# Kernel optimization log

Measured on AMD Instinct MI355X. Metric: run time of the kernel, lower is better.

## Reference

```python
import jax, jax.numpy as jnp
import numpy as np

HIDDEN = 4096
N_HEADS = 32
HEAD_DIM = HIDDEN // N_HEADS  # 128, rotary_dim == head_dim
ROPE_BASE = 10000.0


def apply_rope(x, positions):
    # x: [B, S, n_heads, head_dim]; positions: [B, S] int. GPT-NeoX style (half split).
    hd = x.shape[-1]
    inv_freq = 1.0 / (ROPE_BASE ** (jnp.arange(0, hd, 2, dtype=jnp.float32) / hd))
    freqs = positions.astype(jnp.float32)[..., None] * inv_freq  # [B, S, hd/2]
    cos = jnp.cos(freqs)[:, :, None, :]  # [B, S, 1, hd/2]
    sin = jnp.sin(freqs)[:, :, None, :]
    x1, x2 = jnp.split(x, 2, axis=-1)
    return jnp.concatenate([x1 * cos - x2 * sin, x2 * cos + x1 * sin], axis=-1)


def setup_inputs() -> dict:
    key = jax.random.key(0)
    k1, k2, k3 = jax.random.split(key, 3)
    B, S = 2, 2048
    hidden_states = jax.random.normal(k1, (B, S, HIDDEN), dtype=jnp.float32)
    positions = jnp.broadcast_to(jnp.arange(S, dtype=jnp.int32), (B, S))
    # nn.Linear(hidden, 3*hidden, bias=False): weight [3*hidden, hidden]
    W_pack = jax.random.normal(k2, (3 * HIDDEN, HIDDEN), dtype=jnp.float32) * (HIDDEN ** -0.5)
    W_o = jax.random.normal(k3, (HIDDEN, HIDDEN), dtype=jnp.float32) * (HIDDEN ** -0.5)
    return {"hidden_states": hidden_states, "positions": positions, "W_pack": W_pack, "W_o": W_o}


def reference(hidden_states, positions, W_pack, W_o):
    B, S, H = hidden_states.shape
    scale = HEAD_DIM ** -0.5
    proj = hidden_states @ W_pack.T            # [B, S, 3H]
    q, k, v = jnp.split(proj, 3, axis=-1)
    q = q.reshape(B, S, N_HEADS, HEAD_DIM)
    k = k.reshape(B, S, N_HEADS, HEAD_DIM)
    v = v.reshape(B, S, N_HEADS, HEAD_DIM)
    q = apply_rope(q, positions)
    k = apply_rope(k, positions)
    scores = jnp.einsum("bqnd,bknd->bnqk", q, k) * scale  # [B, n, S, S]
    causal = jnp.tril(jnp.ones((S, S), dtype=bool))
    scores = jnp.where(causal, scores, jnp.finfo(scores.dtype).min)
    probs = jax.nn.softmax(scores, axis=-1)
    attn = jnp.einsum("bnqk,bknd->bqnd", probs, v).reshape(B, S, H)
    return attn @ W_o.T
```

## Files before the change

### kernel.cpp

```cpp
#include <hip/hip_runtime.h>
#include <stdint.h>

#define HIDDEN 4096
#define NHEADS 32
#define HD 128
#define SEQ 2048
#define NTOK 4096
#define QKVN 12288

typedef __attribute__((ext_vector_type(8))) short frag8;
typedef __attribute__((ext_vector_type(4))) float fl4;

__device__ __forceinline__ unsigned short f2b(float f) {
    unsigned u = __float_as_uint(f);
    return (unsigned short)((u + 0x7FFFu + ((u >> 16) & 1u)) >> 16);
}
__device__ __forceinline__ float b2f(unsigned short h) {
    return __uint_as_float(((unsigned)h) << 16);
}
__device__ __forceinline__ void gl_lds16(const void* g, void* l) {
    __builtin_amdgcn_global_load_lds(
        (const __attribute__((address_space(1))) unsigned int*)(uintptr_t)g,
        (__attribute__((address_space(3))) unsigned int*)(uintptr_t)l,
        16, 0, 0);
}

__global__ void cvt_f32_bf16(const float* __restrict__ src,
                             unsigned short* __restrict__ dst, int n8) {
    int i = blockIdx.x * 256 + threadIdx.x;
    if (i >= n8) return;
    long e = (long)i * 8;
    fl4 a = *(const fl4*)(src + e);
    fl4 b = *(const fl4*)(src + e + 4);
    union { unsigned short us[8]; frag8 v; } o;
    o.us[0] = f2b(a[0]); o.us[1] = f2b(a[1]); o.us[2] = f2b(a[2]); o.us[3] = f2b(a[3]);
    o.us[4] = f2b(b[0]); o.us[5] = f2b(b[1]); o.us[6] = f2b(b[2]); o.us[7] = f2b(b[3]);
    *(frag8*)(dst + e) = o.v;
}

__global__ void rope_kernel(unsigned short* __restrict__ proj,
                            const int* __restrict__ positions) {
    int tid = blockIdx.x * 256 + threadIdx.x;
    int j  = tid & 63;
    int h  = (tid >> 6) & 31;
    int qk = (tid >> 11) & 1;
    int t  = tid >> 12;
    int pos = positions[t];
    float inv = __builtin_amdgcn_exp2f(-0.20762051f * (float)j);
    float fr = (float)pos * inv;
    float sv = __sinf(fr), cv = __cosf(fr);
    unsigned short* base = proj + (long)t * QKVN + qk * HIDDEN + h * HD;
    float x1 = b2f(base[j]);
    float x2 = b2f(base[j + 64]);
    base[j]      = f2b(x1 * cv - x2 * sv);
    base[j + 64] = f2b(x2 * cv + x1 * sv);
}

template <int OUT_F32>
__global__ __launch_bounds__(512, 2) void gemm256(
    const unsigned short* __restrict__ A,
    const unsigned short* __restrict__ B,
    void* __restrict__ Cv, int M, int N, int K) {
    __shared__ unsigned short lds[65536];
    const int tid = threadIdx.x, lane = tid & 63, w = tid >> 6;
    const int wr = w >> 2, wc = w & 3;
    const int fr = lane & 15, quad = lane >> 4;

    const int gx = gridDim.x;
    const int nwg = gx * gridDim.y;
    int bid = blockIdx.y * gx + blockIdx.x;
    const int cpx = nwg >> 3;
    int swz = (bid & 7) * cpx + (bid >> 3);
    const long n0 = (long)(swz % gx) * 256;
    const long m0 = (long)(swz / gx) * 256;

    const int r0 = w * 8 + (lane >> 3);
    const int scol = ((lane ^ (lane >> 3)) & 7) * 8;
    const int dofs = w * 512 + lane * 8;
    const unsigned short* Ag = A + (m0 + r0) * (long)K + scol;
    const unsigned short* Bg = B + (n0 + r0) * (long)K + scol;
    auto stg = [&](unsigned short* Lh, const unsigned short* G, long t) {
        gl_lds16(G + t * 64, Lh + dofs);
        gl_lds16(G + t * 64 + (long)K * 64, Lh + dofs + 4096);
    };
#define STGA(s, h, t) stg(lds + (s)*32768 + (h)*8192, Ag + (long)(h) * 128 * K, (t))
#define STGB(s, h, t) stg(lds + (s)*32768 + 16384 + (h)*8192, Bg + (long)(h) * 128 * K, (t))

    const int qx8 = (quad ^ (fr & 3)) * 8;
    const int kx0 = (fr >> 2) & 1;
    const int arow = wr * 64 + fr;
    const int brow = wc * 32 + fr;

    frag8 af[4][2], bf0[2][2], bf1[2][2];
    fl4 acc[2][2][4][2];
    fl4 z = {0.f, 0.f, 0.f, 0.f};
#pragma unroll
    for (int qm = 0; qm < 2; ++qm)
#pragma unroll
        for (int qn = 0; qn < 2; ++qn)
#pragma unroll
            for (int mi = 0; mi < 4; ++mi)
#pragma unroll
                for (int ni = 0; ni < 2; ++ni) acc[qm][qn][mi][ni] = z;

#define LDA(h)                                                                   \
    _Pragma("unroll") for (int mi = 0; mi < 4; ++mi) {                           \
        af[mi][0] = *(const frag8*)(Lc + (h)*8192 + (arow + mi * 16) * 64 +      \
                                    (kx0 << 5) + qx8);                           \
        af[mi][1] = *(const frag8*)(Lc + (h)*8192 + (arow + mi * 16) * 64 +      \
                                    ((1 ^ kx0) << 5) + qx8);                     \
    }
#define LDB(h, BF)                                                               \
    _Pragma("unroll") for (int ni = 0; ni < 2; ++ni) {                           \
        BF[ni][0] = *(const frag8*)(Lc + 16384 + (h)*8192 +                      \
                                    (brow + ni * 16) * 64 + (kx0 << 5) + qx8);   \
        BF[ni][1] = *(const frag8*)(Lc + 16384 + (h)*8192 +                      \
                                    (brow + ni * 16) * 64 + ((1 ^ kx0) << 5) +   \
                                    qx8);                                        \
    }
#define MF(qm, qn, BF)                                                           \
    __builtin_amdgcn_s_setprio(1);                                               \
    _Pragma("unroll") for (int mi = 0; mi < 4; ++mi)                             \
        _Pragma("unroll") for (int ni = 0; ni < 2; ++ni) {                       \
        acc[qm][qn][mi][ni] = __builtin_amdgcn_mfma_f32_16x16x32_bf16(           \
            af[mi][0], BF[ni][0], acc[qm][qn][mi][ni], 0, 0, 0);                 \
        acc[qm][qn][mi][ni] = __builtin_amdgcn_mfma_f32_16x16x32_bf16(           \
            af[mi][1], BF[ni][1], acc[qm][qn][mi][ni], 0, 0, 0);                 \
    }                                                                            \
    __builtin_amdgcn_s_setprio(0);

#define KTILE(s, T)                                                              \
    {                                                                            \
        unsigned short* Lc = lds + (s)*32768;                                    \
        const long t1 = ((T) + 1 < nt) ? (T) + 1 : nt - 1;                       \
        const long t2 = ((T) + 2 < nt) ? (T) + 2 : nt - 1;                       \
        LDA(0);                                                                  \
        LDB(0, bf0);                                                             \
        STGA((s) ^ 1, 1, t1);                                                    \
        __builtin_amdgcn_s_barrier();                                            \
        asm volatile("s_waitcnt lgkmcnt(0)" ::: "memory");                       \
        MF(0, 0, bf0);                                                           \
        __builtin_amdgcn_s_barrier();                                            \
        LDB(1, bf1);                                                             \
        STGA((s), 0, t2);                                                        \
        __builtin_amdgcn_s_barrier();                                            \
        asm volatile("s_waitcnt lgkmcnt(0)" ::: "memory");                       \
        MF(0, 1, bf1);                                                           \
        __builtin_amdgcn_s_barrier();                                            \
        LDA(1);                                                                  \
        STGB((s), 0, t2);                                                        \
        __builtin_amdgcn_s_barrier();                                            \
        asm volatile("s_waitcnt lgkmcnt(0)" ::: "memory");                       \
        MF(1, 0, bf0);                                                           \
        __builtin_amdgcn_s_barrier();                                            \
        STGB((s), 1, t2);                                                        \
        asm volatile("s_waitcnt vmcnt(6)" ::: "memory");                         \
        __builtin_amdgcn_s_barrier();                                            \
        MF(1, 1, bf1);                                                           \
        __builtin_amdgcn_s_barrier();                                            \
    }

    const int nt = K >> 6;
    STGA(0, 0, 0);
    STGB(0, 0, 0);
    STGB(0, 1, 0);
    STGA(0, 1, 0);
    STGA(1, 0, 1);
    STGB(1, 0, 1);
    STGB(1, 1, 1);
    asm volatile("s_waitcnt vmcnt(6)" ::: "memory");
    __builtin_amdgcn_s_barrier();

    for (int T = 0; T < nt; T += 2) {
        KTILE(0, T);
        KTILE(1, T + 1);
    }
    asm volatile("s_waitcnt vmcnt(0)" ::: "memory");

#pragma unroll
    for (int qm = 0; qm < 2; ++qm)
#pragma unroll
        for (int qn = 0; qn < 2; ++qn)
#pragma unroll
            for (int mi = 0; mi < 4; ++mi)
#pragma unroll
                for (int ni = 0; ni < 2; ++ni)
#pragma unroll
                    for (int r = 0; r < 4; ++r) {
                        long row = m0 + qm * 128 + wr * 64 + mi * 16 + quad * 4 + r;
                        long col = n0 + qn * 128 + wc * 32 + ni * 16 + fr;
                        float v = acc[qm][qn][mi][ni][r];
                        if (OUT_F32)
                            ((float*)Cv)[row * N + col] = v;
                        else
                            ((unsigned short*)Cv)[row * N + col] = f2b(v);
                    }
#undef STGA
#undef STGB
#undef LDA
#undef LDB
#undef MF
#undef KTILE
}

__global__ __launch_bounds__(256, 2) void attn_kernel(
    const unsigned short* __restrict__ proj,
    unsigned short* __restrict__ out) {
    __shared__ unsigned short Ks[64 * 128];
    __shared__ unsigned short Vt[128 * 80];
    __shared__ unsigned short Ps[4][32 * 88];

    const int qt = (int)gridDim.x - 1 - (int)blockIdx.x;
    const int h = blockIdx.y;
    const int b = blockIdx.z;
    const int tid = threadIdx.x, lane = tid & 63, w = tid >> 6;
    const int q0 = qt * 128;
    const int fr = lane & 15, quad = lane >> 4;
    const int fq = quad * 8;
    const long tokbase = (long)b * SEQ;
    const float scale = 0.08838834764831845f;
    fl4 z = {0.f, 0.f, 0.f, 0.f};

    frag8 qf[2][4];
#pragma unroll
    for (int mi = 0; mi < 2; mi++)
#pragma unroll
        for (int kc = 0; kc < 4; kc++) {
            int qrow = q0 + w * 32 + mi * 16 + fr;
            qf[mi][kc] = *(const frag8*)(proj + (tokbase + qrow) * QKVN +
                                         h * HD + kc * 32 + fq);
        }

    fl4 o[2][8];
#pragma unroll
    for (int mi = 0; mi < 2; mi++)
#pragma unroll
        for (int n = 0; n < 8; n++) o[mi][n] = z;
    float m_i[2], l_i[2];
    m_i[0] = m_i[1] = -1e30f;
    l_i[0] = l_i[1] = 0.f;

    const int ksrow = w * 4 + (lane >> 4);
    const int kphys = (lane & 15) * 8;
    const int kgcol = ((lane & 15) ^ ksrow) * 8;
    const int vrow = lane;
    const int vdc = w * 32;

    const int ktiles = (q0 + 128) / 64;
    for (int kt = 0; kt < ktiles; kt++) {
        const int k0 = kt * 64;
        __syncthreads();
#pragma unroll
        for (int c = 0; c < 4; c++) {
            long tok = tokbase + k0 + c * 16 + ksrow;
            gl_lds16(proj + tok * QKVN + HIDDEN + h * HD + kgcol,
                     Ks + (c * 16 + ksrow) * 128 + kphys);
        }
        {
            const unsigned short* vp =
                proj + (tokbase + k0 + vrow) * QKVN + 2 * HIDDEN + h * HD + vdc;
#pragma unroll
            for (int u = 0; u < 4; u++) {
                frag8 vv = *(const frag8*)(vp + u * 8);
#pragma unroll
                for (int e = 0; e < 8; e++)
                    Vt[(vdc + u * 8 + e) * 80 + vrow] = (unsigned short)vv[e];
            }
        }
        __syncthreads();

        fl4 sc[2][4];
#pragma unroll
        for (int kn = 0; kn < 4; kn++) {
            frag8 kf[4];
#pragma unroll
            for (int kc = 0; kc < 4; kc++)
                kf[kc] = *(const frag8*)(Ks + (kn * 16 + fr) * 128 +
                                         ((kc * 4 + quad) ^ fr) * 8);
#pragma unroll
            for (int mi = 0; mi < 2; mi++) {
                fl4 a = z;
#pragma unroll
                for (int kc = 0; kc < 4; kc++)
                    a = __builtin_amdgcn_mfma_f32_16x16x32_bf16(kf[kc],
                                                                qf[mi][kc], a, 0, 0, 0);
                sc[mi][kn] = a;
            }
        }

        float mx2[2];
#pragma unroll
        for (int mi = 0; mi < 2; mi++) {
            const int qrow = q0 + w * 32 + mi * 16 + fr;
            float mxv = -1e30f;
#pragma unroll
            for (int kn = 0; kn < 4; kn++) {
                const int kbase = k0 + kn * 16 + quad * 4;
#pragma unroll
                for (int r = 0; r < 4; r++) {
                    float s = sc[mi][kn][r] * scale;
                    s = (kbase + r <= qrow) ? s : -1e30f;
                    sc[mi][kn][r] = s;
                    mxv = fmaxf(mxv, s);
                }
            }
            mxv = fmaxf(mxv, __shfl_xor(mxv, 16, 64));
            mxv = fmaxf(mxv, __shfl_xor(mxv, 32, 64));
            mx2[mi] = mxv;
        }
        bool need = (mx2[0] > m_i[0] + 8.0f) || (mx2[1] > m_i[1] + 8.0f);
        if (__any(need)) {
            float alpha[2];
#pragma unroll
            for (int mi = 0; mi < 2; mi++) {
                float mnew = fmaxf(m_i[mi], mx2[mi]);
                alpha[mi] = __expf(m_i[mi] - mnew);
                m_i[mi] = mnew;
                l_i[mi] *= alpha[mi];
            }
#pragma unroll
            for (int mi = 0; mi < 2; mi++)
#pragma unroll
                for (int rr = 0; rr < 4; rr++) {
                    float af = __shfl(alpha[mi], (lane & 48) | (quad * 4 + rr), 64);
#pragma unroll
                    for (int n = 0; n < 8; n++) o[mi][n][rr] *= af;
                }
        }
#pragma unroll
        for (int mi = 0; mi < 2; mi++) {
            float rsum = 0.f;
            const float m = m_i[mi];
#pragma unroll
            for (int kn = 0; kn < 4; kn++) {
                union { unsigned short us[4]; unsigned long long u; } pk;
#pragma unroll
                for (int r = 0; r < 4; r++) {
                    float p = __expf(sc[mi][kn][r] - m);
                    pk.us[r] = f2b(p);
                    rsum += b2f(pk.us[r]);
                }
                *(unsigned long long*)(&Ps[w][(mi * 16 + fr) * 88 + kn * 16 +
                                              quad * 4]) = pk.u;
            }
            rsum += __shfl_xor(rsum, 16, 64);
            rsum += __shfl_xor(rsum, 32, 64);
            l_i[mi] += rsum;
        }

        frag8 pf[2][2];
#pragma unroll
        for (int mi = 0; mi < 2; mi++)
#pragma unroll
            for (int kc = 0; kc < 2; kc++)
                pf[mi][kc] =
                    *(const frag8*)(Ps[w] + (mi * 16 + fr) * 88 + kc * 32 + fq);
#pragma unroll
        for (int n = 0; n < 8; n++) {
            frag8 vf0 = *(const frag8*)(Vt + (n * 16 + fr) * 80 + fq);
            frag8 vf1 = *(const frag8*)(Vt + (n * 16 + fr) * 80 + 32 + fq);
#pragma unroll
            for (int mi = 0; mi < 2; mi++) {
                o[mi][n] = __builtin_amdgcn_mfma_f32_16x16x32_bf16(pf[mi][0], vf0,
                                                                   o[mi][n], 0, 0, 0);
                o[mi][n] = __builtin_amdgcn_mfma_f32_16x16x32_bf16(pf[mi][1], vf1,
                                                                   o[mi][n], 0, 0, 0);
            }
        }
    }
#pragma unroll
    for (int mi = 0; mi < 2; mi++)
#pragma unroll
        for (int rr = 0; rr < 4; rr++) {
            float lf = __shfl(l_i[mi], (lane & 48) | (quad * 4 + rr), 64);
            float rl = 1.0f / lf;
            int qrow = q0 + w * 32 + mi * 16 + quad * 4 + rr;
#pragma unroll
            for (int n = 0; n < 8; n++)
                out[(tokbase + qrow) * HIDDEN + h * HD + n * 16 + fr] =
                    f2b(o[mi][n][rr] * rl);
        }
}

extern "C" void kernel_launch(void* const* d_in, const int* in_sizes, int n_in,
                              void* d_out, int out_size, void* d_ws, size_t ws_size,
                              hipStream_t stream) {
    const float* hs = (const float*)d_in[0];
    const int* pos  = (const int*)d_in[1];
    const float* wp = (const float*)d_in[2];
    const float* wo = (const float*)d_in[3];
    float* out = (float*)d_out;

    char* ws = (char*)d_ws;
    unsigned short* Xb    = (unsigned short*)ws;
    unsigned short* Wpb   = (unsigned short*)(ws + 33554432L);
    unsigned short* proj  = (unsigned short*)(ws + 134217728L);
    unsigned short* attnb = Wpb;
    unsigned short* Wob   = Xb;

    cvt_f32_bf16<<<(16777216 / 8) / 256, 256, 0, stream>>>(hs, Xb, 16777216 / 8);
    cvt_f32_bf16<<<(50331648 / 8) / 256, 256, 0, stream>>>(wp, Wpb, 50331648 / 8);
    gemm256<0><<<dim3(QKVN / 256, NTOK / 256), 512, 0, stream>>>(
        Xb, Wpb, (void*)proj, NTOK, QKVN, HIDDEN);
    rope_kernel<<<16777216 / 256, 256, 0, stream>>>(proj, pos);
    attn_kernel<<<dim3(SEQ / 128, NHEADS, 2), 256, 0, stream>>>(proj, attnb);
    cvt_f32_bf16<<<(16777216 / 8) / 256, 256, 0, stream>>>(wo, Wob, 16777216 / 8);
    gemm256<1><<<dim3(HIDDEN / 256, NTOK / 256), 512, 0, stream>>>(
        attnb, Wob, d_out, NTOK, HIDDEN, HIDDEN);
}
```

Baseline: 1.091 ms.

## Double-buffer K tiles and prefetch V in attention; regroup GEMM tile swizzle

```diff
diff --git a/kernel.cpp b/kernel.cpp
--- a/kernel.cpp
+++ b/kernel.cpp
@@ -67,12 +67,15 @@
     const int fr = lane & 15, quad = lane >> 4;
 
     const int gx = gridDim.x;
-    const int nwg = gx * gridDim.y;
+    const int gy = gridDim.y;
+    const int nwg = gx * gy;
     int bid = blockIdx.y * gx + blockIdx.x;
     const int cpx = nwg >> 3;
-    int swz = (bid & 7) * cpx + (bid >> 3);
-    const long n0 = (long)(swz % gx) * 256;
-    const long m0 = (long)(swz / gx) * 256;
+    int u = (bid & 7) * cpx + (bid >> 3);
+    int chunk = u >> 5, j = u & 31;
+    const int gy4 = gy >> 2;
+    const long m0 = (long)((chunk % gy4) * 4 + (j >> 3)) * 256;
+    const long n0 = (long)((chunk / gy4) * 8 + (j & 7)) * 256;
 
     const int r0 = w * 8 + (lane >> 3);
     const int scol = ((lane ^ (lane >> 3)) & 7) * 8;
@@ -206,8 +209,8 @@
 __global__ __launch_bounds__(256, 2) void attn_kernel(
     const unsigned short* __restrict__ proj,
     unsigned short* __restrict__ out) {
-    __shared__ unsigned short Ks[64 * 128];
-    __shared__ unsigned short Vt[128 * 80];
+    __shared__ unsigned short Ks[2][64 * 128];
+    __shared__ unsigned short Vt[128 * 82];
     __shared__ unsigned short Ps[4][32 * 88];
 
     const int qt = (int)gridDim.x - 1 - (int)blockIdx.x;
@@ -247,27 +250,46 @@
     const int vdc = w * 32;
 
     const int ktiles = (q0 + 128) / 64;
+
+    frag8 vva[4], vvb[4];
+    {
+#pragma unroll
+        for (int c = 0; c < 4; c++) {
+            long tok = tokbase + 0 + c * 16 + ksrow;
+            gl_lds16(proj + tok * QKVN + HIDDEN + h * HD + kgcol,
+                     Ks[0] + (c * 16 + ksrow) * 128 + kphys);
+        }
+        const unsigned short* vp =
+            proj + (tokbase + 0 + vrow) * QKVN + 2 * HIDDEN + h * HD + vdc;
+#pragma unroll
+        for (int u = 0; u < 4; u++) vva[u] = *(const frag8*)(vp + u * 8);
+    }
+    asm volatile("s_waitcnt vmcnt(0)" ::: "memory");
+    __builtin_amdgcn_s_barrier();
+
+    int cur = 0;
     for (int kt = 0; kt < ktiles; kt++) {
         const int k0 = kt * 64;
-        __syncthreads();
-#pragma unroll
-        for (int c = 0; c < 4; c++) {
-            long tok = tokbase + k0 + c * 16 + ksrow;
-            gl_lds16(proj + tok * QKVN + HIDDEN + h * HD + kgcol,
-                     Ks + (c * 16 + ksrow) * 128 + kphys);
-        }
+#pragma unroll
+        for (int u = 0; u < 4; u++)
+#pragma unroll
+            for (int e = 0; e < 8; e++)
+                Vt[(vdc + u * 8 + e) * 82 + vrow] = (unsigned short)vva[u][e];
         {
+            const int nk0 = (kt + 1 < ktiles) ? (kt + 1) * 64 : kt * 64;
+#pragma unroll
+            for (int c = 0; c < 4; c++) {
+                long tok = tokbase + nk0 + c * 16 + ksrow;
+                gl_lds16(proj + tok * QKVN + HIDDEN + h * HD + kgcol,
+                         Ks[cur ^ 1] + (c * 16 + ksrow) * 128 + kphys);
+            }
             const unsigned short* vp =
-                proj + (tokbase + k0 + vrow) * QKVN + 2 * HIDDEN + h * HD + vdc;
-#pragma unroll
-            for (int u = 0; u < 4; u++) {
-                frag8 vv = *(const frag8*)(vp + u * 8);
-#pragma unroll
-                for (int e = 0; e < 8; e++)
-                    Vt[(vdc + u * 8 + e) * 80 + vrow] = (unsigned short)vv[e];
-            }
-        }
-        __syncthreads();
+                proj + (tokbase + nk0 + vrow) * QKVN + 2 * HIDDEN + h * HD + vdc;
+#pragma unroll
+            for (int u = 0; u < 4; u++) vvb[u] = *(const frag8*)(vp + u * 8);
+        }
+        asm volatile("s_waitcnt lgkmcnt(0)" ::: "memory");
+        __builtin_amdgcn_s_barrier();
 
         fl4 sc[2][4];
 #pragma unroll
@@ -275,7 +297,7 @@
             frag8 kf[4];
 #pragma unroll
             for (int kc = 0; kc < 4; kc++)
-                kf[kc] = *(const frag8*)(Ks + (kn * 16 + fr) * 128 +
+                kf[kc] = *(const frag8*)(Ks[cur] + (kn * 16 + fr) * 128 +
                                          ((kc * 4 + quad) ^ fr) * 8);
 #pragma unroll
             for (int mi = 0; mi < 2; mi++) {
@@ -357,8 +379,8 @@
                     *(const frag8*)(Ps[w] + (mi * 16 + fr) * 88 + kc * 32 + fq);
 #pragma unroll
         for (int n = 0; n < 8; n++) {
-            frag8 vf0 = *(const frag8*)(Vt + (n * 16 + fr) * 80 + fq);
-            frag8 vf1 = *(const frag8*)(Vt + (n * 16 + fr) * 80 + 32 + fq);
+            frag8 vf0 = *(const frag8*)(Vt + (n * 16 + fr) * 82 + fq);
+            frag8 vf1 = *(const frag8*)(Vt + (n * 16 + fr) * 82 + 32 + fq);
 #pragma unroll
             for (int mi = 0; mi < 2; mi++) {
                 o[mi][n] = __builtin_amdgcn_mfma_f32_16x16x32_bf16(pf[mi][0], vf0,
@@ -367,6 +389,11 @@
                                                                    o[mi][n], 0, 0, 0);
             }
         }
+        asm volatile("s_waitcnt vmcnt(0)" ::: "memory");
+        __builtin_amdgcn_s_barrier();
+        cur ^= 1;
+#pragma unroll
+        for (int u = 0; u < 4; u++) vva[u] = vvb[u];
     }
 #pragma unroll
     for (int mi = 0; mi < 2; mi++)
```

Result: faster. 1.042 ms (-4.5%).
